# Kernel tuning notes

Hardware: AMD Instinct MI355X
Metric: run time of the kernel (lower is better)

## Reference

```python
import jax, jax.numpy as jnp
import numpy as np

B, S1, S2 = 4, 2048, 2048
IN1, IN2 = 512, 512
KD, VD, H = 64, 64, 8


def setup_inputs() -> dict:
    key = jax.random.key(0)
    ks = jax.random.split(key, 7)
    x1 = jax.random.normal(ks[0], (B, S1, IN1), dtype=jnp.float32)
    x2 = jax.random.normal(ks[1], (B, S2, IN2), dtype=jnp.float32)
    # nn.Linear weights stored as [out, in]; kaiming-uniform-ish scale
    Wq = jax.random.normal(ks[2], (KD * H, IN1), dtype=jnp.float32) * (1.0 / np.sqrt(IN1))
    Wk = jax.random.normal(ks[3], (KD * H, IN2), dtype=jnp.float32) * (1.0 / np.sqrt(IN2))
    Wv = jax.random.normal(ks[4], (VD * H, IN2), dtype=jnp.float32) * (1.0 / np.sqrt(IN2))
    Wo = jax.random.normal(ks[5], (IN1, VD * H), dtype=jnp.float32) * (1.0 / np.sqrt(VD * H))
    bo = jax.random.normal(ks[6], (IN1,), dtype=jnp.float32) * 0.01
    return {"x1": x1, "x2": x2, "Wq": Wq, "Wk": Wk, "Wv": Wv, "Wo": Wo, "bo": bo}


def reference(x1, x2, Wq, Wk, Wv, Wo, bo):
    b, s1, _ = x1.shape
    s2 = x2.shape[1]
    # projections -> [B, H, S, D]
    q = (x1 @ Wq.T).reshape(b, s1, H, KD).transpose(0, 2, 1, 3)
    k = (x2 @ Wk.T).reshape(b, s2, H, KD).transpose(0, 2, 1, 3)
    v = (x2 @ Wv.T).reshape(b, s2, H, VD).transpose(0, 2, 1, 3)
    # scores [B, H, S1, S2]
    attn = jnp.einsum('bhqd,bhkd->bhqk', q, k) / jnp.sqrt(jnp.float32(KD))
    attn = jax.nn.softmax(attn, axis=-1)
    out = jnp.einsum('bhqk,bhkd->bhqd', attn, v)  # [B, H, S1, VD]
    out = out.transpose(0, 2, 1, 3).reshape(b, s1, H * VD)
    return out @ Wo.T + bo
```

## Files before the change

### kernel.cpp

```cpp
#include <hip/hip_runtime.h>
#include <stdint.h>

typedef __bf16 bf16;
typedef __bf16 bf16x8 __attribute__((ext_vector_type(8)));
typedef __bf16 bf16x4 __attribute__((ext_vector_type(4)));
typedef float f32x4 __attribute__((ext_vector_type(4)));
typedef float f32x16 __attribute__((ext_vector_type(16)));
typedef uint32_t u32x4 __attribute__((ext_vector_type(4)));

#define MFMA16x16x32(A, B, C) __builtin_amdgcn_mfma_f32_16x16x32_bf16((A), (B), (C), 0, 0, 0)
#define MFMA32x32x16(A, B, C) __builtin_amdgcn_mfma_f32_32x32x16_bf16((A), (B), (C), 0, 0, 0)
#define SBAR() do { __builtin_amdgcn_s_barrier(); __builtin_amdgcn_sched_barrier(0); } while (0)

__device__ __forceinline__ void gload_lds16(const void* g, void* l) {
  __builtin_amdgcn_global_load_lds((const __attribute__((address_space(1))) void*)g,
                                   (__attribute__((address_space(3))) void*)l,
                                   16, 0, 0);
}

__device__ __forceinline__ float fexp2(float x) { return __builtin_amdgcn_exp2f(x); }

__device__ __forceinline__ uint32_t cvtpk(float a, float b) {
  uint32_t r;
  asm("v_cvt_pk_bf16_f32 %0, %1, %2" : "=v"(r) : "v"(a), "v"(b));
  return r;
}
__device__ __forceinline__ void plswap(uint32_t& a, uint32_t& b) {
  asm volatile("v_permlane32_swap_b32 %0, %1" : "+v"(a), "+v"(b));
}

__device__ __forceinline__ bf16x8 cvt8(float4 a, float4 b) {
  bf16x8 o;
  o[0] = (bf16)a.x; o[1] = (bf16)a.y; o[2] = (bf16)a.z; o[3] = (bf16)a.w;
  o[4] = (bf16)b.x; o[5] = (bf16)b.y; o[6] = (bf16)b.z; o[7] = (bf16)b.w;
  return o;
}

__global__ void cast_x(const float* __restrict__ x1, const float* __restrict__ x2,
                       const float* __restrict__ Wq, const float* __restrict__ Wk,
                       const float* __restrict__ Wv, const float* __restrict__ Wo,
                       bf16* __restrict__ out) {
  const size_t i = ((size_t)blockIdx.x * blockDim.x + threadIdx.x) * 8;
  const float* src;
  if      (i < 4194304u) src = x1 + i;
  else if (i < 8388608u) src = x2 + (i - 4194304u);
  else if (i < 8650752u) src = Wq + (i - 8388608u);
  else if (i < 8912896u) src = Wk + (i - 8650752u);
  else if (i < 9175040u) src = Wv + (i - 8912896u);
  else                   src = Wo + (i - 9175040u);
  float4 a = *reinterpret_cast<const float4*>(src);
  float4 b = *reinterpret_cast<const float4*>(src + 4);
  *reinterpret_cast<bf16x8*>(out + i) = cvt8(a, b);
}

__global__ __launch_bounds__(256, 3) void qkv128_kernel(
    const bf16* __restrict__ x1b, const bf16* __restrict__ x2b,
    const bf16* __restrict__ Wb, bf16* __restrict__ Qw,
    bf16* __restrict__ Kw, bf16* __restrict__ Vtw) {
  __shared__ bf16 As[3][128 * 32];
  __shared__ bf16 Bs[3][128 * 32];
  const int tid = threadIdx.x;
  const int w = tid >> 6, l = tid & 63;
  const int wr = w >> 1, wc = w & 1;
  const int lr = l & 15, lg = l >> 4;
  const int bm = blockIdx.x, bn = blockIdx.y;
  const int K = 512;
  const int sel = bn >> 2, wn = bn & 3;

  const bf16* A = (sel == 0) ? x1b : x2b;
  const bf16* B = Wb + (size_t)sel * 262144 + (size_t)wn * 128 * K;

  const int c_row = l >> 2;
  const int sw = ((l & 3) ^ (c_row & 3)) * 8;

  auto stage = [&](int t, int bb) {
#pragma unroll
    for (int i = 0; i < 2; i++) {
      const int q = w + i * 4;
      gload_lds16(A + (size_t)(bm * 128 + q * 16 + c_row) * K + t * 32 + sw, &As[bb][q * 512]);
      gload_lds16(B + (size_t)(q * 16 + c_row) * K + t * 32 + sw, &Bs[bb][q * 512]);
    }
  };

  f32x4 acc[4][4] = {};
  const int swz = (lr & 3) * 8;

  stage(0, 0);
  stage(1, 1);
  asm volatile("s_waitcnt vmcnt(4)" ::: "memory");
  SBAR();

  const int NT = 16;
  for (int t = 0; t < NT; t++) {
    if (t + 2 < NT) stage(t + 2, (t + 2) % 3);
    const int cur = t % 3;
    bf16x8 a[4], b[4];
#pragma unroll
    for (int mi = 0; mi < 4; mi++)
      a[mi] = *reinterpret_cast<const bf16x8*>(
          &As[cur][(wr * 64 + mi * 16 + lr) * 32 + (lg * 8 ^ swz)]);
#pragma unroll
    for (int ni = 0; ni < 4; ni++)
      b[ni] = *reinterpret_cast<const bf16x8*>(
          &Bs[cur][(wc * 64 + ni * 16 + lr) * 32 + (lg * 8 ^ swz)]);
#pragma unroll
    for (int mi = 0; mi < 4; mi++)
#pragma unroll
      for (int ni = 0; ni < 4; ni++)
        acc[mi][ni] = MFMA16x16x32(a[mi], b[ni], acc[mi][ni]);

    if (t + 1 < NT) {
      if (t + 2 < NT) asm volatile("s_waitcnt vmcnt(4)" ::: "memory");
      else            asm volatile("s_waitcnt vmcnt(0)" ::: "memory");
      asm volatile("s_waitcnt lgkmcnt(0)" ::: "memory");
      SBAR();
    }
  }

  const float scale = (sel == 0) ? 0.18033688011112f : 1.0f;
#pragma unroll
  for (int mi = 0; mi < 4; mi++) {
    const int m0 = bm * 128 + wr * 64 + mi * 16 + lg * 4;
#pragma unroll
    for (int ni = 0; ni < 4; ni++) {
      const int gn = wn * 128 + wc * 64 + ni * 16 + lr;
      if (sel < 2) {
        bf16* dst = (sel == 0) ? Qw : Kw;
#pragma unroll
        for (int r = 0; r < 4; r++) {
          const int m = m0 + r;
          size_t d = (size_t)((m >> 11) * 8 + (gn >> 6)) * 131072 + (size_t)(m & 2047) * 64 + (gn & 63);
          dst[d] = (bf16)(acc[mi][ni][r] * scale);
        }
      } else {
        bf16x4 pv;
#pragma unroll
        for (int r = 0; r < 4; r++) pv[r] = (bf16)acc[mi][ni][r];
        size_t base = ((size_t)(m0 >> 11) * 512 + gn) * 2048 + (m0 & 2047);
        *reinterpret_cast<bf16x4*>(Vtw + base) = pv;
      }
    }
  }
}

__global__ __launch_bounds__(256, 4) void outproj_kernel(
    const bf16* __restrict__ A0, const float* __restrict__ W0,
    float* __restrict__ C0, const float* __restrict__ bias) {
  __shared__ bf16 As[3][128 * 32];
  __shared__ bf16 Bs[2][64 * 32];
  const int tid = threadIdx.x;
  const int w = tid >> 6, l = tid & 63;
  const int wr = w >> 1, wc = w & 1;
  const int lr = l & 15, lg = l >> 4;
  const int bm = blockIdx.x, bn = blockIdx.y;
  const int K = 512;

  const float* Bf = W0 + (size_t)bn * 64 * K;
  const int c_row = l >> 2;
  const int c_s = l & 3;
  const int sw = (c_s ^ (c_row & 3)) * 8;

  float4 lb[2][2];
  auto issue_A = [&](int t, int bb) {
#pragma unroll
    for (int i = 0; i < 2; i++) {
      const int q = w + i * 4;
      gload_lds16(A0 + (size_t)(bm * 128 + q * 16 + c_row) * K + t * 32 + sw, &As[bb][q * 512]);
    }
  };
  auto issue_B = [&](int t, int s) {
    const float* pb = Bf + (size_t)(w * 16 + c_row) * K + t * 32 + c_s * 8;
    lb[s][0] = *reinterpret_cast<const float4*>(pb);
    lb[s][1] = *reinterpret_cast<const float4*>(pb + 4);
  };
  auto commit_B = [&](int s, int bb) {
    *reinterpret_cast<bf16x8*>(&Bs[bb][w * 512 + c_row * 32 + sw]) = cvt8(lb[s][0], lb[s][1]);
  };

  f32x4 acc[4][2] = {};
  const int swz = (lr & 3) * 8;

  issue_A(0, 0); issue_B(0, 0);
  issue_A(1, 1); issue_B(1, 1);
  asm volatile("s_waitcnt vmcnt(4)" ::: "memory");
  commit_B(0, 0);
  asm volatile("s_waitcnt lgkmcnt(0)" ::: "memory");
  SBAR();

  const int NT = 16;
  for (int t = 0; t < NT; t++) {
    if (t + 2 < NT) { issue_A(t + 2, (t + 2) % 3); issue_B(t + 2, t & 1); }

    bf16x8 a[4], b[2];
    const int cur = t % 3;
#pragma unroll
    for (int mi = 0; mi < 4; mi++)
      a[mi] = *reinterpret_cast<const bf16x8*>(
          &As[cur][(wr * 64 + mi * 16 + lr) * 32 + (lg * 8 ^ swz)]);
#pragma unroll
    for (int ni = 0; ni < 2; ni++)
      b[ni] = *reinterpret_cast<const bf16x8*>(
          &Bs[t & 1][(wc * 32 + ni * 16 + lr) * 32 + (lg * 8 ^ swz)]);
#pragma unroll
    for (int mi = 0; mi < 4; mi++)
#pragma unroll
      for (int ni = 0; ni < 2; ni++)
        acc[mi][ni] = MFMA16x16x32(a[mi], b[ni], acc[mi][ni]);

    if (t + 1 < NT) {
      if (t + 2 < NT) asm volatile("s_waitcnt vmcnt(4)" ::: "memory");
      else            asm volatile("s_waitcnt vmcnt(0)" ::: "memory");
      commit_B((t + 1) & 1, (t + 1) & 1);
      asm volatile("s_waitcnt lgkmcnt(0)" ::: "memory");
      SBAR();
    }
  }

#pragma unroll
  for (int mi = 0; mi < 4; mi++) {
    const int m0 = bm * 128 + wr * 64 + mi * 16 + lg * 4;
#pragma unroll
    for (int ni = 0; ni < 2; ni++) {
      const int gn = bn * 64 + wc * 32 + ni * 16 + lr;
      const float bv = bias[gn];
#pragma unroll
      for (int r = 0; r < 4; r++)
        C0[(size_t)(m0 + r) * 512 + gn] = acc[mi][ni][r] + bv;
    }
  }
}

__global__ __launch_bounds__(512, 1) void attn_kernel(
    const bf16* __restrict__ Q, const bf16* __restrict__ Kk,
    const bf16* __restrict__ Vt, bf16* __restrict__ AO) {
  __shared__ bf16 KV[2][2][64 * 64];
  __shared__ float cls[4][2][32];

  const int tid = threadIdx.x;
  const int w = tid >> 6, l = tid & 63;
  const int q32 = l & 31;
  const int h = l >> 5;
  const int qg = w >> 1, kvh = w & 1;

  const int lin = blockIdx.x;
  const int xcd = lin & 7;
  const int m = lin >> 3;
  const int bh = xcd * 4 + (m & 3);
  const int qb = m >> 2;
  const int b = bh >> 3, hd = bh & 7;

  const bf16* Qb = Q + (size_t)bh * 131072;
  const bf16* Kb = Kk + (size_t)bh * 131072;
  const bf16* Vb = Vt + (size_t)bh * 131072;

  const int q0 = qb * 256 + qg * 64;

  bf16x8 qf[2][4];
#pragma unroll
  for (int i = 0; i < 2; i++)
#pragma unroll
    for (int ks = 0; ks < 4; ks++)
      qf[i][ks] = *reinterpret_cast<const bf16x8*>(
          Qb + (size_t)(q0 + i * 32 + q32) * 64 + ks * 16 + h * 8);

  const int crow = l >> 3;
  const int scol = ((l & 7) ^ crow) * 8;
  auto stage = [&](int kv0, int bb) {
    const int row = w * 8 + crow;
    gload_lds16(Kb + (size_t)(kv0 + row) * 64 + scol, &KV[0][bb][w * 512]);
    gload_lds16(Vb + (size_t)row * 2048 + kv0 + scol, &KV[1][bb][w * 512]);
  };

  f32x16 oacc[2][2] = {};
  float lsum[2] = {0.f, 0.f};
  const int l7 = l & 7;

  stage(0, 0);
  asm volatile("s_waitcnt vmcnt(0)" ::: "memory");
  SBAR();

  for (int t = 0; t < 32; t++) {
    const int cur = t & 1;
    if (t < 31) stage((t + 1) * 64, cur ^ 1);

    bf16x8 kb[4];
#pragma unroll
    for (int ks = 0; ks < 4; ks++)
      kb[ks] = *reinterpret_cast<const bf16x8*>(
          &KV[0][cur][(kvh * 32 + q32) * 64 + (((ks * 2 + h) ^ l7) * 8)]);

    bf16x8 pa[2][2];
#pragma unroll
    for (int i = 0; i < 2; i++) {
      f32x16 st = {};
#pragma unroll
      for (int ks = 0; ks < 4; ks++)
        st = MFMA32x32x16(kb[ks], qf[i][ks], st);

      float e[16];
#pragma unroll
      for (int r = 0; r < 16; r++) {
        e[r] = fexp2(st[r]);
        lsum[i] += e[r];
      }
      uint32_t Qp[8];
#pragma unroll
      for (int p = 0; p < 8; p++) Qp[p] = cvtpk(e[2 * p], e[2 * p + 1]);
      plswap(Qp[0], Qp[2]);
      plswap(Qp[1], Qp[3]);
      plswap(Qp[4], Qp[6]);
      plswap(Qp[5], Qp[7]);
      pa[i][0] = __builtin_bit_cast(bf16x8, (u32x4){Qp[0], Qp[1], Qp[2], Qp[3]});
      pa[i][1] = __builtin_bit_cast(bf16x8, (u32x4){Qp[4], Qp[5], Qp[6], Qp[7]});
    }

    bf16x8 vb[2][2];
#pragma unroll
    for (int kst = 0; kst < 2; kst++)
#pragma unroll
      for (int db = 0; db < 2; db++)
        vb[kst][db] = *reinterpret_cast<const bf16x8*>(
            &KV[1][cur][(db * 32 + q32) * 64 + (((kvh * 4 + kst * 2 + h) ^ l7) * 8)]);

#pragma unroll
    for (int i = 0; i < 2; i++)
#pragma unroll
      for (int kst = 0; kst < 2; kst++)
#pragma unroll
        for (int db = 0; db < 2; db++)
          oacc[i][db] = MFMA32x32x16(pa[i][kst], vb[kst][db], oacc[i][db]);

    if (t < 31) {
      asm volatile("s_waitcnt vmcnt(0) lgkmcnt(0)" ::: "memory");
      SBAR();
    }
  }

#pragma unroll
  for (int i = 0; i < 2; i++) lsum[i] += __shfl_xor(lsum[i], 32);

  float* cb = (float*)&KV[0][0][0];
  __syncthreads();
  if (kvh == 1 && l < 32) {
    cls[qg][0][q32] = lsum[0];
    cls[qg][1][q32] = lsum[1];
  }
#pragma unroll
  for (int i = 0; i < 2; i++) {
    if (kvh == 1) {
#pragma unroll
      for (int db = 0; db < 2; db++)
#pragma unroll
        for (int r = 0; r < 16; r++)
          cb[((qg * 2 + db) * 16 + r) * 64 + l] = oacc[i][db][r];
    }
    __syncthreads();
    if (kvh == 0) {
#pragma unroll
      for (int db = 0; db < 2; db++)
#pragma unroll
        for (int r = 0; r < 16; r++)
          oacc[i][db][r] += cb[((qg * 2 + db) * 16 + r) * 64 + l];
    }
    __syncthreads();
  }

  if (kvh == 0) {
#pragma unroll
    for (int i = 0; i < 2; i++) {
      lsum[i] += cls[qg][i][q32];
      float inv[16];
#pragma unroll
      for (int r = 0; r < 16; r++) {
        const int qv = (r & 3) + 8 * (r >> 2) + 4 * h;
        inv[r] = 1.f / __shfl(lsum[i], qv);
      }
#pragma unroll
      for (int db = 0; db < 2; db++) {
#pragma unroll
        for (int r = 0; r < 16; r++) {
          const int qv = (r & 3) + 8 * (r >> 2) + 4 * h;
          AO[(size_t)(b * 2048 + q0 + i * 32 + qv) * 512 + hd * 64 + db * 32 + q32] =
              (bf16)(oacc[i][db][r] * inv[r]);
        }
      }
    }
  }
}

extern "C" void kernel_launch(void* const* d_in, const int* in_sizes, int n_in,
                              void* d_out, int out_size, void* d_ws, size_t ws_size,
                              hipStream_t stream) {
  (void)in_sizes; (void)n_in; (void)out_size; (void)ws_size;
  const float* x1 = (const float*)d_in[0];
  const float* x2 = (const float*)d_in[1];
  const float* Wq = (const float*)d_in[2];
  const float* Wk = (const float*)d_in[3];
  const float* Wv = (const float*)d_in[4];
  const float* Wo = (const float*)d_in[5];
  const float* bo = (const float*)d_in[6];

  uint8_t* ws = (uint8_t*)d_ws;
  bf16* x1b = (bf16*)(ws + 0);
  bf16* x2b = (bf16*)(ws + 8388608);
  bf16* Wsb = (bf16*)(ws + 16777216);
  bf16* AO  = (bf16*)(ws + 0);
  bf16* Qws = (bf16*)(ws + 18874368);
  bf16* Kws = (bf16*)(ws + 27262976);
  bf16* Vtw = (bf16*)(ws + 35651584);

  cast_x<<<4608, 256, 0, stream>>>(x1, x2, Wq, Wk, Wv, Wo, x1b);

  qkv128_kernel<<<dim3(64, 12), 256, 0, stream>>>(x1b, x2b, Wsb, Qws, Kws, Vtw);

  attn_kernel<<<256, 512, 0, stream>>>(Qws, Kws, Vtw, AO);

  outproj_kernel<<<dim3(64, 8), 256, 0, stream>>>(AO, Wo, (float*)d_out, bo);
}
```

Measured before the change: 97.01 us.

## Fuse fp32-to-bf16 cast into QKV GEMM loads and prioritise attention MFMA

Removes the standalone cast kernel. The QKV projection GEMM now reads fp32 activations and weights into registers, converts them to bf16 and writes the swizzled tiles to LDS in a register-staged, double-issue pipeline instead of using direct global-to-LDS loads. This saves a full pass of reads and writes over x1/x2 and an extra launch. The cost is doubled global bytes per GEMM tile, more registers (launch bounds lowered to 2) and VALU conversion work inside the main loop. The attention kernel also raises wave priority around its MFMA section.

```diff
diff --git a/kernel.cpp b/kernel.cpp
--- a/kernel.cpp
+++ b/kernel.cpp
@@ -36,26 +36,10 @@
   return o;
 }
 
-__global__ void cast_x(const float* __restrict__ x1, const float* __restrict__ x2,
-                       const float* __restrict__ Wq, const float* __restrict__ Wk,
-                       const float* __restrict__ Wv, const float* __restrict__ Wo,
-                       bf16* __restrict__ out) {
-  const size_t i = ((size_t)blockIdx.x * blockDim.x + threadIdx.x) * 8;
-  const float* src;
-  if      (i < 4194304u) src = x1 + i;
-  else if (i < 8388608u) src = x2 + (i - 4194304u);
-  else if (i < 8650752u) src = Wq + (i - 8388608u);
-  else if (i < 8912896u) src = Wk + (i - 8650752u);
-  else if (i < 9175040u) src = Wv + (i - 8912896u);
-  else                   src = Wo + (i - 9175040u);
-  float4 a = *reinterpret_cast<const float4*>(src);
-  float4 b = *reinterpret_cast<const float4*>(src + 4);
-  *reinterpret_cast<bf16x8*>(out + i) = cvt8(a, b);
-}
-
-__global__ __launch_bounds__(256, 3) void qkv128_kernel(
-    const bf16* __restrict__ x1b, const bf16* __restrict__ x2b,
-    const bf16* __restrict__ Wb, bf16* __restrict__ Qw,
+__global__ __launch_bounds__(256, 2) void qkv128_kernel(
+    const float* __restrict__ x1, const float* __restrict__ x2,
+    const float* __restrict__ Wq, const float* __restrict__ Wk,
+    const float* __restrict__ Wv, bf16* __restrict__ Qw,
     bf16* __restrict__ Kw, bf16* __restrict__ Vtw) {
   __shared__ bf16 As[3][128 * 32];
   __shared__ bf16 Bs[3][128 * 32];
@@ -67,33 +51,40 @@
   const int K = 512;
   const int sel = bn >> 2, wn = bn & 3;
 
-  const bf16* A = (sel == 0) ? x1b : x2b;
-  const bf16* B = Wb + (size_t)sel * 262144 + (size_t)wn * 128 * K;
+  const float* A = (sel == 0) ? x1 : x2;
+  const float* B = ((sel == 0) ? Wq : (sel == 1) ? Wk : Wv) + (size_t)wn * 128 * K;
 
   const int c_row = l >> 2;
-  const int sw = ((l & 3) ^ (c_row & 3)) * 8;
-
-  auto stage = [&](int t, int bb) {
-#pragma unroll
-    for (int i = 0; i < 2; i++) {
-      const int q = w + i * 4;
-      gload_lds16(A + (size_t)(bm * 128 + q * 16 + c_row) * K + t * 32 + sw, &As[bb][q * 512]);
-      gload_lds16(B + (size_t)(q * 16 + c_row) * K + t * 32 + sw, &Bs[bb][q * 512]);
-    }
-  };
+  const int c_s = l & 3;
+  const int sw = (c_s ^ (c_row & 3)) * 8;
+
+  float4 ra0[2][2], ra1[2][2], rb0[2][2], rb1[2][2];
+
+#define ISSUE(t, ra, rb)                                                          \
+  {                                                                               \
+    _Pragma("unroll") for (int i = 0; i < 2; i++) {                               \
+      const int q = w + i * 4;                                                    \
+      const float* pa = A + (size_t)(bm * 128 + q * 16 + c_row) * K + (t) * 32 + c_s * 8; \
+      ra[i][0] = *reinterpret_cast<const float4*>(pa);                            \
+      ra[i][1] = *reinterpret_cast<const float4*>(pa + 4);                        \
+      const float* pb = B + (size_t)(q * 16 + c_row) * K + (t) * 32 + c_s * 8;    \
+      rb[i][0] = *reinterpret_cast<const float4*>(pb);                            \
+      rb[i][1] = *reinterpret_cast<const float4*>(pb + 4);                        \
+    }                                                                             \
+  }
+#define COMMIT(bb, ra, rb)                                                        \
+  {                                                                               \
+    _Pragma("unroll") for (int i = 0; i < 2; i++) {                               \
+      const int q = w + i * 4;                                                    \
+      *reinterpret_cast<bf16x8*>(&As[bb][q * 512 + c_row * 32 + sw]) = cvt8(ra[i][0], ra[i][1]); \
+      *reinterpret_cast<bf16x8*>(&Bs[bb][q * 512 + c_row * 32 + sw]) = cvt8(rb[i][0], rb[i][1]); \
+    }                                                                             \
+  }
 
   f32x4 acc[4][4] = {};
   const int swz = (lr & 3) * 8;
 
-  stage(0, 0);
-  stage(1, 1);
-  asm volatile("s_waitcnt vmcnt(4)" ::: "memory");
-  SBAR();
-
-  const int NT = 16;
-  for (int t = 0; t < NT; t++) {
-    if (t + 2 < NT) stage(t + 2, (t + 2) % 3);
-    const int cur = t % 3;
+  auto compute = [&](int cur) {
     bf16x8 a[4], b[4];
 #pragma unroll
     for (int mi = 0; mi < 4; mi++)
@@ -108,14 +99,38 @@
 #pragma unroll
       for (int ni = 0; ni < 4; ni++)
         acc[mi][ni] = MFMA16x16x32(a[mi], b[ni], acc[mi][ni]);
-
-    if (t + 1 < NT) {
-      if (t + 2 < NT) asm volatile("s_waitcnt vmcnt(4)" ::: "memory");
+  };
+
+  ISSUE(0, ra0, rb0);
+  ISSUE(1, ra1, rb1);
+  asm volatile("s_waitcnt vmcnt(8)" ::: "memory");
+  COMMIT(0, ra0, rb0);
+  asm volatile("s_waitcnt lgkmcnt(0)" ::: "memory");
+  SBAR();
+
+  const int NT = 16;
+  for (int t = 0; t < NT; t += 2) {
+    if (t + 2 < NT) ISSUE(t + 2, ra0, rb0);
+    compute(t % 3);
+    {
+      if (t + 2 < NT) asm volatile("s_waitcnt vmcnt(8)" ::: "memory");
       else            asm volatile("s_waitcnt vmcnt(0)" ::: "memory");
+      COMMIT((t + 1) % 3, ra1, rb1);
       asm volatile("s_waitcnt lgkmcnt(0)" ::: "memory");
       SBAR();
     }
-  }
+    if (t + 3 < NT) ISSUE(t + 3, ra1, rb1);
+    compute((t + 1) % 3);
+    if (t + 2 < NT) {
+      if (t + 3 < NT) asm volatile("s_waitcnt vmcnt(8)" ::: "memory");
+      else            asm volatile("s_waitcnt vmcnt(0)" ::: "memory");
+      COMMIT((t + 2) % 3, ra0, rb0);
+      asm volatile("s_waitcnt lgkmcnt(0)" ::: "memory");
+      SBAR();
+    }
+  }
+#undef ISSUE
+#undef COMMIT
 
   const float scale = (sel == 0) ? 0.18033688011112f : 1.0f;
 #pragma unroll
@@ -283,6 +298,8 @@
     const int cur = t & 1;
     if (t < 31) stage((t + 1) * 64, cur ^ 1);
 
+    __builtin_amdgcn_s_setprio(1);
+
     bf16x8 kb[4];
 #pragma unroll
     for (int ks = 0; ks < 4; ks++)
@@ -329,6 +346,8 @@
 #pragma unroll
         for (int db = 0; db < 2; db++)
           oacc[i][db] = MFMA32x32x16(pa[i][kst], vb[kst][db], oacc[i][db]);
+
+    __builtin_amdgcn_s_setprio(0);
 
     if (t < 31) {
       asm volatile("s_waitcnt vmcnt(0) lgkmcnt(0)" ::: "memory");
@@ -401,17 +420,12 @@
   const float* bo = (const float*)d_in[6];
 
   uint8_t* ws = (uint8_t*)d_ws;
-  bf16* x1b = (bf16*)(ws + 0);
-  bf16* x2b = (bf16*)(ws + 8388608);
-  bf16* Wsb = (bf16*)(ws + 16777216);
   bf16* AO  = (bf16*)(ws + 0);
   bf16* Qws = (bf16*)(ws + 18874368);
   bf16* Kws = (bf16*)(ws + 27262976);
   bf16* Vtw = (bf16*)(ws + 35651584);
 
-  cast_x<<<4608, 256, 0, stream>>>(x1, x2, Wq, Wk, Wv, Wo, x1b);
-
-  qkv128_kernel<<<dim3(64, 12), 256, 0, stream>>>(x1b, x2b, Wsb, Qws, Kws, Vtw);
+  qkv128_kernel<<<dim3(64, 12), 256, 0, stream>>>(x1, x2, Wq, Wk, Wv, Qws, Kws, Vtw);
 
   attn_kernel<<<256, 512, 0, stream>>>(Qws, Kws, Vtw, AO);
 
```

Result: no change. 96.74 us (-0.3%).
